# Performance work log

Measured on AMD Instinct MI355X. Metric: run time of the kernel, lower is better.

The kernel has to match this reference:

```python
import jax, jax.numpy as jnp
import numpy as np

RAD = 0.15          # sphere radius (init kwarg)
MIN_DIST = 2.0 * RAD  # two spheres collide when center distance < 2*rad


def setup_inputs() -> dict:
    key = jax.random.key(0)
    pos = jax.random.normal(key, (64, 1024, 3), dtype=jnp.float32)  # [T, N, 3]
    return {"pos": pos}


def reference(pos):
    """Sphere collision check equivalent to the sweep-and-prune CUDA kernel.

    The CUDA kernel sorts along one axis purely as an acceleration structure;
    the math it computes is: over all unordered robot pairs (i<j) at each
    timestep, a pair collides if ||p_i - p_j|| < 2*rad. Returns
      count: total number of colliding pairs (int)
      loss:  sum over colliding pairs of (2*rad - dist)^2 penetration penalty
    """
    T, N, _ = pos.shape
    diff = pos[:, :, None, :] - pos[:, None, :, :]          # [T, N, N, 3]
    dist2 = jnp.sum(diff * diff, axis=-1)                   # [T, N, N]
    iu = jnp.triu(jnp.ones((N, N), dtype=bool), k=1)        # i < j, exclude self
    colliding = iu[None, :, :] & (dist2 < MIN_DIST * MIN_DIST)
    # safe sqrt (diagonal / coincident points have dist2 == 0)
    safe_d2 = jnp.where(dist2 > 0.0, dist2, 1.0)
    dist = jnp.sqrt(safe_d2)
    pen = MIN_DIST - dist                                   # penetration depth
    loss = jnp.sum(jnp.where(colliding, pen * pen, 0.0))
    count = jnp.sum(colliding).astype(jnp.int32)
    return (count, loss)
```

## Files before the change

### kernel.cpp

```cpp
#include <hip/hip_runtime.h>
#include <math.h>

#define TN     64
#define NP     1024
#define RADIUS 0.15f
#define MIN_D  (2.0f * RADIUS)
#define R2     (MIN_D * MIN_D)

#define SPLIT  16
#define GI     16
#define NGRP   (NP / GI)
#define GPB    (NGRP / SPLIT)
#define BLOCK  256
#define NBLK   (TN * SPLIT)

__launch_bounds__(BLOCK, 4)
__global__ void collide_kernel(const float* __restrict__ pos,
                               float* __restrict__ partial) {
    __shared__ float sh[NP * 3];
    const int t     = blockIdx.x / SPLIT;
    const int split = blockIdx.x % SPLIT;
    const int tid   = threadIdx.x;

    const float4* p4  = (const float4*)(pos + (size_t)t * NP * 3);
    float4*       sh4 = (float4*)sh;
    #pragma unroll
    for (int i = 0; i < (NP * 3 / 4) / BLOCK; ++i)
        sh4[tid + i * BLOCK] = p4[tid + i * BLOCK];
    __syncthreads();

    unsigned int cnt = 0;
    float loss = 0.0f;

    #pragma unroll
    for (int m = 0; m < GPB; ++m) {
        const int g = (m & 1) ? (m * SPLIT + (SPLIT - 1 - split))
                              : (m * SPLIT + split);
        const int b = g * GI;

        float xi[GI], yi[GI], zi[GI];
        #pragma unroll
        for (int k = 0; k < GI; ++k) {
            xi[k] = sh[3 * (b + k) + 0];
            yi[k] = sh[3 * (b + k) + 1];
            zi[k] = sh[3 * (b + k) + 2];
        }
        #pragma unroll
        for (int k = 0; k < GI; ++k)
            asm volatile("" : "+v"(xi[k]), "+v"(yi[k]), "+v"(zi[k]));

        if (tid < GI - 1) {
            const int j = b + 1 + tid;
            const float xj = sh[3 * j], yj = sh[3 * j + 1], zj = sh[3 * j + 2];
            #pragma unroll
            for (int k = 0; k < GI; ++k) {
                if (k <= tid) {
                    const float dx = xi[k] - xj;
                    const float dy = yi[k] - yj;
                    const float dz = zi[k] - zj;
                    const float d2 = dx * dx + dy * dy + dz * dz;
                    cnt += (d2 < R2) ? 1u : 0u;
                    const float pen = fmaxf(MIN_D - __builtin_amdgcn_sqrtf(d2), 0.0f);
                    loss += pen * pen;
                }
            }
        }

        #pragma unroll 2
        for (int j = b + GI + tid; j < NP; j += BLOCK) {
            const float xj = sh[3 * j], yj = sh[3 * j + 1], zj = sh[3 * j + 2];
            #pragma unroll
            for (int k = 0; k < GI; ++k) {
                const float dx = xi[k] - xj;
                const float dy = yi[k] - yj;
                const float dz = zi[k] - zj;
                const float d2 = dx * dx + dy * dy + dz * dz;
                cnt += (d2 < R2) ? 1u : 0u;
                const float pen = fmaxf(MIN_D - __builtin_amdgcn_sqrtf(d2), 0.0f);
                loss += pen * pen;
            }
        }
    }

    float fcnt = (float)cnt;
    #pragma unroll
    for (int off = 32; off > 0; off >>= 1) {
        fcnt += __shfl_down(fcnt, off);
        loss += __shfl_down(loss, off);
    }
    __shared__ float cs[BLOCK / 64], ls[BLOCK / 64];
    const int wave = tid >> 6;
    if ((tid & 63) == 0) { cs[wave] = fcnt; ls[wave] = loss; }
    __syncthreads();
    if (tid == 0) {
        float c = 0.0f, l = 0.0f;
        #pragma unroll
        for (int w = 0; w < BLOCK / 64; ++w) { c += cs[w]; l += ls[w]; }
        partial[2 * blockIdx.x + 0] = c;
        partial[2 * blockIdx.x + 1] = l;
    }
}

__global__ void finalize_kernel(const float* __restrict__ partial,
                                float* __restrict__ out) {
    const int tid = threadIdx.x;
    float c = 0.0f, l = 0.0f;
    #pragma unroll
    for (int i = 0; i < NBLK / BLOCK; ++i) {
        const float2 p = ((const float2*)partial)[tid + i * BLOCK];
        c += p.x;
        l += p.y;
    }
    #pragma unroll
    for (int off = 32; off > 0; off >>= 1) {
        c += __shfl_down(c, off);
        l += __shfl_down(l, off);
    }
    __shared__ float cs[BLOCK / 64], ls[BLOCK / 64];
    const int wave = tid >> 6;
    if ((tid & 63) == 0) { cs[wave] = c; ls[wave] = l; }
    __syncthreads();
    if (tid == 0) {
        float ct = 0.0f, lt = 0.0f;
        #pragma unroll
        for (int w = 0; w < BLOCK / 64; ++w) { ct += cs[w]; lt += ls[w]; }
        out[0] = ct;
        out[1] = lt;
    }
}

extern "C" void kernel_launch(void* const* d_in, const int* in_sizes, int n_in,
                              void* d_out, int out_size, void* d_ws, size_t ws_size,
                              hipStream_t stream) {
    const float* pos     = (const float*)d_in[0];
    float*       partial = (float*)d_ws;
    float*       out     = (float*)d_out;

    collide_kernel<<<NBLK, BLOCK, 0, stream>>>(pos, partial);
    finalize_kernel<<<1, BLOCK, 0, stream>>>(partial, out);
}
```

Baseline: 73.37 us.

## Pad positions to float4 in LDS, halve group size, stop unrolling outer loop

Stores each position as a padded float4 in shared memory, so a j-point needs one 128-bit LDS read instead of three scalar reads. The i-group size drops from 16 to 8, which doubles the number of groups each block walks, and the outer group loop is no longer unrolled, to cut code size and register pressure. The trade-off is more passes over shared memory per pair, less register reuse, and 33% more LDS footprint.

Result: slower. 76.99 us (+4.9%).

```diff
diff --git a/kernel.cpp b/kernel.cpp
--- a/kernel.cpp
+++ b/kernel.cpp
@@ -8,7 +8,7 @@
 #define R2     (MIN_D * MIN_D)
 
 #define SPLIT  16
-#define GI     16
+#define GI     8
 #define NGRP   (NP / GI)
 #define GPB    (NGRP / SPLIT)
 #define BLOCK  256
@@ -17,22 +17,28 @@
 __launch_bounds__(BLOCK, 4)
 __global__ void collide_kernel(const float* __restrict__ pos,
                                float* __restrict__ partial) {
-    __shared__ float sh[NP * 3];
-    const int t     = blockIdx.x / SPLIT;
-    const int split = blockIdx.x % SPLIT;
+    __shared__ float4 shp[NP];
+    const int bid   = blockIdx.x;
+    const int t     = bid / SPLIT;
+    const int split = bid % SPLIT;
     const int tid   = threadIdx.x;
 
-    const float4* p4  = (const float4*)(pos + (size_t)t * NP * 3);
-    float4*       sh4 = (float4*)sh;
-    #pragma unroll
-    for (int i = 0; i < (NP * 3 / 4) / BLOCK; ++i)
-        sh4[tid + i * BLOCK] = p4[tid + i * BLOCK];
+    {
+        const float4* p4 = (const float4*)(pos + (size_t)t * NP * 3);
+        const float4 a = p4[3 * tid + 0];
+        const float4 b = p4[3 * tid + 1];
+        const float4 c = p4[3 * tid + 2];
+        shp[4 * tid + 0] = make_float4(a.x, a.y, a.z, 0.0f);
+        shp[4 * tid + 1] = make_float4(a.w, b.x, b.y, 0.0f);
+        shp[4 * tid + 2] = make_float4(b.z, b.w, c.x, 0.0f);
+        shp[4 * tid + 3] = make_float4(c.y, c.z, c.w, 0.0f);
+    }
     __syncthreads();
 
     unsigned int cnt = 0;
     float loss = 0.0f;
 
-    #pragma unroll
+    #pragma unroll 1
     for (int m = 0; m < GPB; ++m) {
         const int g = (m & 1) ? (m * SPLIT + (SPLIT - 1 - split))
                               : (m * SPLIT + split);
@@ -41,23 +47,21 @@
         float xi[GI], yi[GI], zi[GI];
         #pragma unroll
         for (int k = 0; k < GI; ++k) {
-            xi[k] = sh[3 * (b + k) + 0];
-            yi[k] = sh[3 * (b + k) + 1];
-            zi[k] = sh[3 * (b + k) + 2];
+            const float4 pk = shp[b + k];
+            xi[k] = pk.x; yi[k] = pk.y; zi[k] = pk.z;
         }
         #pragma unroll
         for (int k = 0; k < GI; ++k)
             asm volatile("" : "+v"(xi[k]), "+v"(yi[k]), "+v"(zi[k]));
 
         if (tid < GI - 1) {
-            const int j = b + 1 + tid;
-            const float xj = sh[3 * j], yj = sh[3 * j + 1], zj = sh[3 * j + 2];
+            const float4 pj = shp[b + 1 + tid];
             #pragma unroll
             for (int k = 0; k < GI; ++k) {
                 if (k <= tid) {
-                    const float dx = xi[k] - xj;
-                    const float dy = yi[k] - yj;
-                    const float dz = zi[k] - zj;
+                    const float dx = xi[k] - pj.x;
+                    const float dy = yi[k] - pj.y;
+                    const float dz = zi[k] - pj.z;
                     const float d2 = dx * dx + dy * dy + dz * dz;
                     cnt += (d2 < R2) ? 1u : 0u;
                     const float pen = fmaxf(MIN_D - __builtin_amdgcn_sqrtf(d2), 0.0f);
@@ -66,14 +70,13 @@
             }
         }
 
-        #pragma unroll 2
         for (int j = b + GI + tid; j < NP; j += BLOCK) {
-            const float xj = sh[3 * j], yj = sh[3 * j + 1], zj = sh[3 * j + 2];
+            const float4 pj = shp[j];
             #pragma unroll
             for (int k = 0; k < GI; ++k) {
-                const float dx = xi[k] - xj;
-                const float dy = yi[k] - yj;
-                const float dz = zi[k] - zj;
+                const float dx = xi[k] - pj.x;
+                const float dy = yi[k] - pj.y;
+                const float dz = zi[k] - pj.z;
                 const float d2 = dx * dx + dy * dy + dz * dz;
                 cnt += (d2 < R2) ? 1u : 0u;
                 const float pen = fmaxf(MIN_D - __builtin_amdgcn_sqrtf(d2), 0.0f);
@@ -96,8 +99,8 @@
         float c = 0.0f, l = 0.0f;
         #pragma unroll
         for (int w = 0; w < BLOCK / 64; ++w) { c += cs[w]; l += ls[w]; }
-        partial[2 * blockIdx.x + 0] = c;
-        partial[2 * blockIdx.x + 1] = l;
+        partial[2 * bid + 0] = c;
+        partial[2 * bid + 1] = l;
     }
 }
 
```
